# Kernel optimization log

Hardware: AMD Instinct MI355X
Metric: run time of the kernel (lower is better)

Reference implementation:

```python
import jax, jax.numpy as jnp
import numpy as np

N_NODES = 50000
N_EDGES = 800000
IN_FEATS = 128
HIDDEN = 96
NUM_CLASSES = 21
LEAKY_SLOPE = 0.01  # torch F.leaky_relu default


def setup_inputs() -> dict:
    key = jax.random.key(0)
    ks = jax.random.split(key, 12)
    x = jax.random.normal(ks[0], (N_NODES, IN_FEATS), dtype=jnp.float32)
    edge_index = jax.random.randint(ks[1], (2, N_EDGES), 0, N_NODES, dtype=jnp.int64)

    def glorot(k, fan_in, fan_out):
        lim = np.sqrt(6.0 / (fan_in + fan_out)).astype(np.float32)
        return jax.random.uniform(k, (fan_in, fan_out), jnp.float32, -lim, lim)

    return {
        "x": x,
        "edge_index": edge_index,
        "W1": glorot(ks[2], IN_FEATS, HIDDEN), "b1": jnp.zeros((HIDDEN,), jnp.float32),
        "W2": glorot(ks[3], HIDDEN, HIDDEN),   "b2": jnp.zeros((HIDDEN,), jnp.float32),
        "W3": glorot(ks[4], HIDDEN, HIDDEN),   "b3": jnp.zeros((HIDDEN,), jnp.float32),
        "Wl": glorot(ks[5], HIDDEN, NUM_CLASSES), "bl": jnp.zeros((NUM_CLASSES,), jnp.float32),
    }


def _gcn_norm(edge_index, num_nodes):
    # Add self-loops (PyG GCNConv default) and compute symmetric normalization
    loop = jnp.arange(num_nodes, dtype=edge_index.dtype)
    src = jnp.concatenate([edge_index[0], loop])  # source j
    tgt = jnp.concatenate([edge_index[1], loop])  # target i (aggregation index)
    ones = jnp.ones(src.shape[0], dtype=jnp.float32)
    deg = jax.ops.segment_sum(ones, tgt, num_segments=num_nodes)  # in-degree incl. self-loop
    dinv = jnp.where(deg > 0, jax.lax.rsqrt(deg), 0.0)
    norm = dinv[src] * dinv[tgt]  # [E+N]
    return src, tgt, norm


def _gcn_conv(h, src, tgt, norm, W, b, num_nodes):
    h = h @ W                                   # [N, out] dense transform first
    msg = norm[:, None] * h[src]                # gather + scale, [E+N, out]
    out = jax.ops.segment_sum(msg, tgt, num_segments=num_nodes)  # scatter-add
    return out + b


def reference(x, edge_index, W1, b1, W2, b2, W3, b3, Wl, bl):
    n = x.shape[0]
    src, tgt, norm = _gcn_norm(edge_index, n)
    # dropout is a no-op in eval mode (training=False)
    h = jax.nn.leaky_relu(_gcn_conv(x, src, tgt, norm, W1, b1, n), LEAKY_SLOPE)
    h = jax.nn.leaky_relu(_gcn_conv(h, src, tgt, norm, W2, b2, n), LEAKY_SLOPE)
    h = jax.nn.leaky_relu(_gcn_conv(h, src, tgt, norm, W3, b3, n), LEAKY_SLOPE)
    return h @ Wl + bl  # [N, num_classes]
```

## Files before the change

### kernel.cpp

```cpp
#include <hip/hip_runtime.h>
#include <hip/hip_fp16.h>

#define N_NODES 50000
#define N_EDGES 800000
#define IN_F 128
#define HID 96
#define NCLS 21
#define NBUCK 196
#define BCAP  4608
#define CPAD  16

typedef _Float16 hvec2 __attribute__((ext_vector_type(2)));

__device__ __forceinline__ float fdot2f(__half2 a, __half2 b, float c) {
#if __has_builtin(__builtin_amdgcn_fdot2)
  union { __half2 h; hvec2 v; } ua, ub;
  ua.h = a; ub.h = b;
  return __builtin_amdgcn_fdot2(ua.v, ub.v, c, false);
#else
  float2 fa = __half22float2(a), fb = __half22float2(b);
  return c + fa.x * fb.x + fa.y * fb.y;
#endif
}

__global__ void k_zero_int(int* __restrict__ p, int n) {
  int i = blockIdx.x * blockDim.x + threadIdx.x;
  if (i < n) p[i] = 0;
}

__global__ __launch_bounds__(1024) void k_bin(
    const int* __restrict__ src, const int* __restrict__ tgt,
    int* __restrict__ cursor, int* __restrict__ packed) {
  __shared__ int lhist[NBUCK];
  __shared__ int gbase[NBUCK];
  int tid = threadIdx.x;
  if (tid < NBUCK) lhist[tid] = 0;
  __syncthreads();
  int me = blockIdx.x * 4096 + tid * 4;
  int4 t4, s4;
  int b0 = 0, b1 = 0, b2 = 0, b3 = 0;
  bool valid = me < N_EDGES;
  if (valid) {
    t4 = *reinterpret_cast<const int4*>(tgt + me);
    s4 = *reinterpret_cast<const int4*>(src + me);
    b0 = t4.x >> 8; b1 = t4.y >> 8; b2 = t4.z >> 8; b3 = t4.w >> 8;
    atomicAdd(&lhist[b0], 1); atomicAdd(&lhist[b1], 1);
    atomicAdd(&lhist[b2], 1); atomicAdd(&lhist[b3], 1);
  }
  __syncthreads();
  if (tid < NBUCK) {
    int c = lhist[tid];
    gbase[tid] = c ? atomicAdd(&cursor[tid * CPAD], c) : 0;
    lhist[tid] = 0;
  }
  __syncthreads();
  if (valid) {
    int r, pos;
    r = atomicAdd(&lhist[b0], 1);
    pos = gbase[b0] + r;
    if (pos < BCAP) packed[b0 * BCAP + pos] = (s4.x << 8) | (t4.x & 255);
    r = atomicAdd(&lhist[b1], 1);
    pos = gbase[b1] + r;
    if (pos < BCAP) packed[b1 * BCAP + pos] = (s4.y << 8) | (t4.y & 255);
    r = atomicAdd(&lhist[b2], 1);
    pos = gbase[b2] + r;
    if (pos < BCAP) packed[b2 * BCAP + pos] = (s4.z << 8) | (t4.z & 255);
    r = atomicAdd(&lhist[b3], 1);
    pos = gbase[b3] + r;
    if (pos < BCAP) packed[b3 * BCAP + pos] = (s4.w << 8) | (t4.w & 255);
  }
}

__global__ __launch_bounds__(256) void k_build(
    const int* __restrict__ cursor, const int* __restrict__ packed,
    int* __restrict__ adj, int* __restrict__ degarr,
    int* __restrict__ rowptr, float* __restrict__ dinv) {
  __shared__ int ncnt[256];
  __shared__ int noff[256];
  __shared__ int nrank[256];
  __shared__ int ws[4];
  int b = blockIdx.x;
  int tid = threadIdx.x;
  int cntb = cursor[b * CPAD];
  if (cntb > BCAP) cntb = BCAP;
  ncnt[tid] = 0;
  nrank[tid] = 0;
  __syncthreads();
  const int* pk = packed + b * BCAP;
  for (int i = tid; i < cntb; i += 256) atomicAdd(&ncnt[pk[i] & 255], 1);
  __syncthreads();
  {
    int lane = tid & 63, wid = tid >> 6;
    int v = ncnt[tid];
    int x = v;
#pragma unroll
    for (int off = 1; off < 64; off <<= 1) {
      int y = __shfl_up(x, off);
      if (lane >= off) x += y;
    }
    if (lane == 63) ws[wid] = x;
    __syncthreads();
    if (tid == 0) {
      int t0 = ws[0], t1 = ws[1], t2 = ws[2];
      ws[3] = t0 + t1 + t2; ws[2] = t0 + t1; ws[1] = t0; ws[0] = 0;
    }
    __syncthreads();
    noff[tid] = ws[wid] + x - v;
  }
  __syncthreads();
  int n = (b << 8) + tid;
  if (n < N_NODES) {
    int d = ncnt[tid];
    degarr[n] = d;
    rowptr[n] = b * BCAP + noff[tid];
    dinv[n] = rsqrtf(1.0f + (float)d);
  }
  __syncthreads();
  for (int i = tid; i < cntb; i += 256) {
    int e = pk[i];
    int low = e & 255;
    int r = atomicAdd(&nrank[low], 1);
    adj[b * BCAP + noff[low] + r] = e >> 8;
  }
}

template<int K, bool A_HALF>
__global__ __launch_bounds__(128) void k_gemm_dot2(
    const void* __restrict__ Av, const float* __restrict__ W,
    const float* __restrict__ dinv, __half* __restrict__ g) {
  constexpr int BM = 64;
  constexpr int KP = 16;
  __shared__ __half2 As2[KP][BM + 2];
  __shared__ __half2 Ws2[KP][HID];
  int tid = threadIdx.x;
  int tx = tid & 15;
  int ty = tid >> 4;
  int f0 = tx * 6;
  int nbase = blockIdx.x * BM;
  float acc[8][6] = {};

  for (int k0 = 0; k0 < K; k0 += 32) {
    if (A_HALF) {
      const __half* A = (const __half*)Av;
#pragma unroll
      for (int i = 0; i < 2; i++) {
        int l = tid + i * 128;
        int row = l >> 2;
        int col8 = (l & 3) * 8;
        int n = nbase + row;
        uint4 v = make_uint4(0u, 0u, 0u, 0u);
        if (n < N_NODES)
          v = *reinterpret_cast<const uint4*>(A + (size_t)n * HID + k0 + col8);
        int p = col8 >> 1;
        As2[p + 0][row] = *(const __half2*)&v.x;
        As2[p + 1][row] = *(const __half2*)&v.y;
        As2[p + 2][row] = *(const __half2*)&v.z;
        As2[p + 3][row] = *(const __half2*)&v.w;
      }
    } else {
      const float* A = (const float*)Av;
#pragma unroll
      for (int i = 0; i < 4; i++) {
        int l = tid + i * 128;
        int row = l >> 3;
        int col = (l & 7) * 4;
        int n = nbase + row;
        float4 a4 = make_float4(0.f, 0.f, 0.f, 0.f);
        if (n < N_NODES)
          a4 = *reinterpret_cast<const float4*>(A + (size_t)n * K + k0 + col);
        As2[(col >> 1) + 0][row] = __floats2half2_rn(a4.x, a4.y);
        As2[(col >> 1) + 1][row] = __floats2half2_rn(a4.z, a4.w);
      }
    }
#pragma unroll
    for (int i = 0; i < 3; i++) {
      int l = tid + i * 128;
      int r2 = l / 24;
      int c4 = (l % 24) * 4;
      const float* w0 = W + (size_t)(k0 + 2 * r2) * HID + c4;
      float4 wa = *reinterpret_cast<const float4*>(w0);
      float4 wb = *reinterpret_cast<const float4*>(w0 + HID);
      Ws2[r2][c4 + 0] = __floats2half2_rn(wa.x, wb.x);
      Ws2[r2][c4 + 1] = __floats2half2_rn(wa.y, wb.y);
      Ws2[r2][c4 + 2] = __floats2half2_rn(wa.z, wb.z);
      Ws2[r2][c4 + 3] = __floats2half2_rn(wa.w, wb.w);
    }
    __syncthreads();
#pragma unroll
    for (int k2 = 0; k2 < KP; k2++) {
      __half2 av[8], wv[6];
#pragma unroll
      for (int i = 0; i < 8; i++) av[i] = As2[k2][ty * 8 + i];
#pragma unroll
      for (int j = 0; j < 6; j++) wv[j] = Ws2[k2][f0 + j];
#pragma unroll
      for (int i = 0; i < 8; i++)
#pragma unroll
        for (int j = 0; j < 6; j++) acc[i][j] = fdot2f(av[i], wv[j], acc[i][j]);
    }
    __syncthreads();
  }

#pragma unroll
  for (int i = 0; i < 8; i++) {
    int n = nbase + ty * 8 + i;
    if (n >= N_NODES) break;
    float d = dinv[n];
    __half2* gp = reinterpret_cast<__half2*>(g + (size_t)n * HID + f0);
#pragma unroll
    for (int j = 0; j < 3; j++)
      gp[j] = __floats2half2_rn(acc[i][2 * j] * d, acc[i][2 * j + 1] * d);
  }
}

__global__ __launch_bounds__(128) void k_aggregate(
    const __half* __restrict__ g, const int* __restrict__ degarr,
    const int* __restrict__ rowptr, const int* __restrict__ adj,
    const float* __restrict__ dinv, const float* __restrict__ b,
    __half* __restrict__ hout) {
  int n = blockIdx.x * 2 + (threadIdx.x >> 6);
  if (n >= N_NODES) return;
  int lane = threadIdx.x & 63;
  bool act = lane < 48;
  int deg = degarr[n];
  const int* al = adj + rowptr[n];
  int myidx = (lane < deg) ? al[lane] : 0;

  const char* gb = (const char*)g;
  int loff = lane * 4;
  float sx, sy;
  {
    unsigned v = act ? *(const unsigned*)(gb + (size_t)n * 192 + loff) : 0u;
    float2 t = __half22float2(*(const __half2*)&v);
    sx = t.x; sy = t.y;
  }

  int dd = deg > 64 ? 64 : deg;
  int j = 0;
  for (; j + 16 <= dd; j += 16) {
    unsigned v[16];
#pragma unroll
    for (int u = 0; u < 16; u++) {
      int idx = __shfl(myidx, j + u);
      v[u] = act ? *(const unsigned*)(gb + (size_t)idx * 192 + loff) : 0u;
    }
#pragma unroll
    for (int u = 0; u < 16; u++) {
      float2 t = __half22float2(*(const __half2*)&v[u]);
      sx += t.x; sy += t.y;
    }
  }
  if (j + 8 <= dd) {
    unsigned v[8];
#pragma unroll
    for (int u = 0; u < 8; u++) {
      int idx = __shfl(myidx, j + u);
      v[u] = act ? *(const unsigned*)(gb + (size_t)idx * 192 + loff) : 0u;
    }
#pragma unroll
    for (int u = 0; u < 8; u++) {
      float2 t = __half22float2(*(const __half2*)&v[u]);
      sx += t.x; sy += t.y;
    }
    j += 8;
  }
  if (j + 4 <= dd) {
    unsigned v[4];
#pragma unroll
    for (int u = 0; u < 4; u++) {
      int idx = __shfl(myidx, j + u);
      v[u] = act ? *(const unsigned*)(gb + (size_t)idx * 192 + loff) : 0u;
    }
#pragma unroll
    for (int u = 0; u < 4; u++) {
      float2 t = __half22float2(*(const __half2*)&v[u]);
      sx += t.x; sy += t.y;
    }
    j += 4;
  }
  for (; j < dd; j++) {
    int idx = __shfl(myidx, j);
    unsigned v = act ? *(const unsigned*)(gb + (size_t)idx * 192 + loff) : 0u;
    float2 t = __half22float2(*(const __half2*)&v);
    sx += t.x; sy += t.y;
  }
  for (; j < deg; j++) {
    int idx = al[j];
    unsigned v = act ? *(const unsigned*)(gb + (size_t)idx * 192 + loff) : 0u;
    float2 t = __half22float2(*(const __half2*)&v);
    sx += t.x; sy += t.y;
  }

  if (act) {
    float d = dinv[n];
    float2 bb = *reinterpret_cast<const float2*>(b + 2 * lane);
    float v0 = d * sx + bb.x;
    float v1 = d * sy + bb.y;
    v0 = v0 > 0.f ? v0 : 0.01f * v0;
    v1 = v1 > 0.f ? v1 : 0.01f * v1;
    *reinterpret_cast<__half2*>(hout + (size_t)n * HID + 2 * lane) =
        __floats2half2_rn(v0, v1);
  }
}

__global__ __launch_bounds__(256) void k_final(
    const __half* __restrict__ H, const float* __restrict__ Wl,
    const float* __restrict__ bl, float* __restrict__ out) {
  __shared__ __half2 w2[HID / 2][NCLS];
  __shared__ float bs[NCLS];
  int tid = threadIdx.x;
  for (int i = tid; i < (HID / 2) * NCLS; i += 256) {
    int r2 = i / NCLS;
    int c = i - r2 * NCLS;
    w2[r2][c] = __floats2half2_rn(Wl[(size_t)(2 * r2) * NCLS + c],
                                  Wl[(size_t)(2 * r2 + 1) * NCLS + c]);
  }
  if (tid < NCLS) bs[tid] = bl[tid];
  __syncthreads();
  int idx = blockIdx.x * 256 + tid;
  if (idx >= N_NODES * NCLS) return;
  int n = idx / NCLS;
  int c = idx - n * NCLS;
  const __half2* a2 = reinterpret_cast<const __half2*>(H + (size_t)n * HID);
  float s = bs[c];
#pragma unroll
  for (int k2 = 0; k2 < HID / 2; k2++) s = fdot2f(a2[k2], w2[k2][c], s);
  out[idx] = s;
}

extern "C" void kernel_launch(void* const* d_in, const int* in_sizes, int n_in,
                              void* d_out, int out_size, void* d_ws, size_t ws_size,
                              hipStream_t stream) {
  const float* x  = (const float*)d_in[0];
  const int* ei   = (const int*)d_in[1];
  const int* src  = ei;
  const int* tgt  = ei + N_EDGES;
  const float* W1 = (const float*)d_in[2];
  const float* b1 = (const float*)d_in[3];
  const float* W2 = (const float*)d_in[4];
  const float* b2 = (const float*)d_in[5];
  const float* W3 = (const float*)d_in[6];
  const float* b3 = (const float*)d_in[7];
  const float* Wl = (const float*)d_in[8];
  const float* bl = (const float*)d_in[9];
  float* out = (float*)d_out;

  float*  dinv   = (float*)d_ws;
  __half* bufG   = (__half*)(dinv + N_NODES);
  __half* bufH   = bufG + (size_t)N_NODES * HID;
  int*    degarr = (int*)(bufH + (size_t)N_NODES * HID);
  int*    rowptr = degarr + N_NODES;
  int*    cursor = rowptr + N_NODES;
  int*    packed = cursor + NBUCK * CPAD;
  int*    adj    = packed + NBUCK * BCAP;

  k_zero_int<<<(NBUCK * CPAD + 255) / 256, 256, 0, stream>>>(cursor, NBUCK * CPAD);
  k_bin<<<(N_EDGES + 4095) / 4096, 1024, 0, stream>>>(src, tgt, cursor, packed);
  k_build<<<NBUCK, 256, 0, stream>>>(cursor, packed, adj, degarr, rowptr, dinv);

  const int ggrid = (N_NODES + 63) / 64;
  const int agrid = (N_NODES + 1) / 2;

  k_gemm_dot2<IN_F, false><<<ggrid, 128, 0, stream>>>(x, W1, dinv, bufG);
  k_aggregate<<<agrid, 128, 0, stream>>>(bufG, degarr, rowptr, adj, dinv, b1, bufH);
  k_gemm_dot2<HID, true><<<ggrid, 128, 0, stream>>>(bufH, W2, dinv, bufG);
  k_aggregate<<<agrid, 128, 0, stream>>>(bufG, degarr, rowptr, adj, dinv, b2, bufH);
  k_gemm_dot2<HID, true><<<ggrid, 128, 0, stream>>>(bufH, W3, dinv, bufG);
  k_aggregate<<<agrid, 128, 0, stream>>>(bufG, degarr, rowptr, adj, dinv, b3, bufH);

  k_final<<<(N_NODES * NCLS + 255) / 256, 256, 0, stream>>>(bufH, Wl, bl, out);
}
```

Measured before the change: 196.4 us.

## Switch dense GEMM to MFMA f16 and use nontemporal gathers in aggregation

Replaces the packed-half dot2 GEMM with a 256-thread kernel in which each wave computes a 16-row tile using the 16x16x32 f16 MFMA across six column blocks, with A and transposed W staged in LDS. The aim is to move the dense transforms onto the matrix cores and cut their ALU time. The output stores become scattered 2-byte writes, and W is transposed with scalar loads on every k-step, which may add memory overhead. Neighbor gathers in the aggregation kernel also switch to nontemporal loads, which changes cache behaviour for a gather that is reused across many nodes and could hurt L2 reuse.

```diff
diff --git a/kernel.cpp b/kernel.cpp
--- a/kernel.cpp
+++ b/kernel.cpp
@@ -11,6 +11,8 @@
 #define CPAD  16
 
 typedef _Float16 hvec2 __attribute__((ext_vector_type(2)));
+typedef _Float16 f16x8 __attribute__((ext_vector_type(8)));
+typedef float f32x4 __attribute__((ext_vector_type(4)));
 
 __device__ __forceinline__ float fdot2f(__half2 a, __half2 b, float c) {
 #if __has_builtin(__builtin_amdgcn_fdot2)
@@ -125,91 +127,74 @@
 }
 
 template<int K, bool A_HALF>
-__global__ __launch_bounds__(128) void k_gemm_dot2(
+__global__ __launch_bounds__(256) void k_gemm_mfma(
     const void* __restrict__ Av, const float* __restrict__ W,
     const float* __restrict__ dinv, __half* __restrict__ g) {
   constexpr int BM = 64;
-  constexpr int KP = 16;
-  __shared__ __half2 As2[KP][BM + 2];
-  __shared__ __half2 Ws2[KP][HID];
+  constexpr int LDA = 40;
+  __shared__ _Float16 As[BM][LDA];
+  __shared__ _Float16 Wt[HID][LDA];
   int tid = threadIdx.x;
-  int tx = tid & 15;
-  int ty = tid >> 4;
-  int f0 = tx * 6;
+  int wave = tid >> 6;
+  int lane = tid & 63;
   int nbase = blockIdx.x * BM;
-  float acc[8][6] = {};
+  f32x4 acc[6] = {};
 
   for (int k0 = 0; k0 < K; k0 += 32) {
-    if (A_HALF) {
-      const __half* A = (const __half*)Av;
-#pragma unroll
-      for (int i = 0; i < 2; i++) {
-        int l = tid + i * 128;
-        int row = l >> 2;
-        int col8 = (l & 3) * 8;
-        int n = nbase + row;
+    {
+      int row = tid >> 2;
+      int c8 = (tid & 3) * 8;
+      int n = nbase + row;
+      if (A_HALF) {
+        const __half* A = (const __half*)Av;
         uint4 v = make_uint4(0u, 0u, 0u, 0u);
-        if (n < N_NODES)
-          v = *reinterpret_cast<const uint4*>(A + (size_t)n * HID + k0 + col8);
-        int p = col8 >> 1;
-        As2[p + 0][row] = *(const __half2*)&v.x;
-        As2[p + 1][row] = *(const __half2*)&v.y;
-        As2[p + 2][row] = *(const __half2*)&v.z;
-        As2[p + 3][row] = *(const __half2*)&v.w;
+        if (n < N_NODES) v = *reinterpret_cast<const uint4*>(A + (size_t)n * K + k0 + c8);
+        *reinterpret_cast<uint4*>(&As[row][c8]) = v;
+      } else {
+        const float* A = (const float*)Av;
+        float4 a0 = make_float4(0.f, 0.f, 0.f, 0.f), a1 = a0;
+        if (n < N_NODES) {
+          a0 = *reinterpret_cast<const float4*>(A + (size_t)n * K + k0 + c8);
+          a1 = *reinterpret_cast<const float4*>(A + (size_t)n * K + k0 + c8 + 4);
+        }
+        f16x8 hv;
+        hv[0] = (_Float16)a0.x; hv[1] = (_Float16)a0.y;
+        hv[2] = (_Float16)a0.z; hv[3] = (_Float16)a0.w;
+        hv[4] = (_Float16)a1.x; hv[5] = (_Float16)a1.y;
+        hv[6] = (_Float16)a1.z; hv[7] = (_Float16)a1.w;
+        *reinterpret_cast<f16x8*>(&As[row][c8]) = hv;
       }
-    } else {
-      const float* A = (const float*)Av;
-#pragma unroll
-      for (int i = 0; i < 4; i++) {
-        int l = tid + i * 128;
-        int row = l >> 3;
-        int col = (l & 7) * 4;
-        int n = nbase + row;
-        float4 a4 = make_float4(0.f, 0.f, 0.f, 0.f);
-        if (n < N_NODES)
-          a4 = *reinterpret_cast<const float4*>(A + (size_t)n * K + k0 + col);
-        As2[(col >> 1) + 0][row] = __floats2half2_rn(a4.x, a4.y);
-        As2[(col >> 1) + 1][row] = __floats2half2_rn(a4.z, a4.w);
+    }
+#pragma unroll
+    for (int i = 0; i < 12; i++) {
+      int idx = tid + i * 256;
+      int col = idx % HID;
+      int k = idx / HID;
+      Wt[col][k] = (_Float16)W[(size_t)(k0 + k) * HID + col];
+    }
+    __syncthreads();
+    {
+      f16x8 a = *reinterpret_cast<const f16x8*>(&As[wave * 16 + (lane & 15)][(lane >> 4) * 8]);
+#pragma unroll
+      for (int cb = 0; cb < 6; cb++) {
+        f16x8 b = *reinterpret_cast<const f16x8*>(&Wt[cb * 16 + (lane & 15)][(lane >> 4) * 8]);
+        acc[cb] = __builtin_amdgcn_mfma_f32_16x16x32_f16(a, b, acc[cb], 0, 0, 0);
       }
     }
-#pragma unroll
-    for (int i = 0; i < 3; i++) {
-      int l = tid + i * 128;
-      int r2 = l / 24;
-      int c4 = (l % 24) * 4;
-      const float* w0 = W + (size_t)(k0 + 2 * r2) * HID + c4;
-      float4 wa = *reinterpret_cast<const float4*>(w0);
-      float4 wb = *reinterpret_cast<const float4*>(w0 + HID);
-      Ws2[r2][c4 + 0] = __floats2half2_rn(wa.x, wb.x);
-      Ws2[r2][c4 + 1] = __floats2half2_rn(wa.y, wb.y);
-      Ws2[r2][c4 + 2] = __floats2half2_rn(wa.z, wb.z);
-      Ws2[r2][c4 + 3] = __floats2half2_rn(wa.w, wb.w);
-    }
     __syncthreads();
-#pragma unroll
-    for (int k2 = 0; k2 < KP; k2++) {
-      __half2 av[8], wv[6];
-#pragma unroll
-      for (int i = 0; i < 8; i++) av[i] = As2[k2][ty * 8 + i];
-#pragma unroll
-      for (int j = 0; j < 6; j++) wv[j] = Ws2[k2][f0 + j];
-#pragma unroll
-      for (int i = 0; i < 8; i++)
-#pragma unroll
-        for (int j = 0; j < 6; j++) acc[i][j] = fdot2f(av[i], wv[j], acc[i][j]);
-    }
-    __syncthreads();
-  }
-
-#pragma unroll
-  for (int i = 0; i < 8; i++) {
-    int n = nbase + ty * 8 + i;
-    if (n >= N_NODES) break;
-    float d = dinv[n];
-    __half2* gp = reinterpret_cast<__half2*>(g + (size_t)n * HID + f0);
-#pragma unroll
-    for (int j = 0; j < 3; j++)
-      gp[j] = __floats2half2_rn(acc[i][2 * j] * d, acc[i][2 * j + 1] * d);
+  }
+
+#pragma unroll
+  for (int r = 0; r < 4; r++) {
+    int row = wave * 16 + (lane >> 4) * 4 + r;
+    int n = nbase + row;
+    if (n < N_NODES) {
+      float d = dinv[n];
+      __half* gp = g + (size_t)n * HID + (lane & 15);
+#pragma unroll
+      for (int cb = 0; cb < 6; cb++)
+        gp[cb * 16] = __float2half(acc[cb][r] * d);
+    }
   }
 }
 
@@ -230,7 +215,8 @@
   int loff = lane * 4;
   float sx, sy;
   {
-    unsigned v = act ? *(const unsigned*)(gb + (size_t)n * 192 + loff) : 0u;
+    unsigned v = act ? __builtin_nontemporal_load(
+                           (const unsigned*)(gb + (size_t)n * 192 + loff)) : 0u;
     float2 t = __half22float2(*(const __half2*)&v);
     sx = t.x; sy = t.y;
   }
@@ -242,7 +228,8 @@
 #pragma unroll
     for (int u = 0; u < 16; u++) {
       int idx = __shfl(myidx, j + u);
-      v[u] = act ? *(const unsigned*)(gb + (size_t)idx * 192 + loff) : 0u;
+      v[u] = act ? __builtin_nontemporal_load(
+                       (const unsigned*)(gb + (size_t)idx * 192 + loff)) : 0u;
     }
 #pragma unroll
     for (int u = 0; u < 16; u++) {
@@ -255,7 +242,8 @@
 #pragma unroll
     for (int u = 0; u < 8; u++) {
       int idx = __shfl(myidx, j + u);
-      v[u] = act ? *(const unsigned*)(gb + (size_t)idx * 192 + loff) : 0u;
+      v[u] = act ? __builtin_nontemporal_load(
+                       (const unsigned*)(gb + (size_t)idx * 192 + loff)) : 0u;
     }
 #pragma unroll
     for (int u = 0; u < 8; u++) {
@@ -269,7 +257,8 @@
 #pragma unroll
     for (int u = 0; u < 4; u++) {
       int idx = __shfl(myidx, j + u);
-      v[u] = act ? *(const unsigned*)(gb + (size_t)idx * 192 + loff) : 0u;
+      v[u] = act ? __builtin_nontemporal_load(
+                       (const unsigned*)(gb + (size_t)idx * 192 + loff)) : 0u;
     }
 #pragma unroll
     for (int u = 0; u < 4; u++) {
@@ -280,13 +269,15 @@
   }
   for (; j < dd; j++) {
     int idx = __shfl(myidx, j);
-    unsigned v = act ? *(const unsigned*)(gb + (size_t)idx * 192 + loff) : 0u;
+    unsigned v = act ? __builtin_nontemporal_load(
+                           (const unsigned*)(gb + (size_t)idx * 192 + loff)) : 0u;
     float2 t = __half22float2(*(const __half2*)&v);
     sx += t.x; sy += t.y;
   }
   for (; j < deg; j++) {
     int idx = al[j];
-    unsigned v = act ? *(const unsigned*)(gb + (size_t)idx * 192 + loff) : 0u;
+    unsigned v = act ? __builtin_nontemporal_load(
+                           (const unsigned*)(gb + (size_t)idx * 192 + loff)) : 0u;
     float2 t = __half22float2(*(const __half2*)&v);
     sx += t.x; sy += t.y;
   }
@@ -361,11 +352,11 @@
   const int ggrid = (N_NODES + 63) / 64;
   const int agrid = (N_NODES + 1) / 2;
 
-  k_gemm_dot2<IN_F, false><<<ggrid, 128, 0, stream>>>(x, W1, dinv, bufG);
+  k_gemm_mfma<IN_F, false><<<ggrid, 256, 0, stream>>>(x, W1, dinv, bufG);
   k_aggregate<<<agrid, 128, 0, stream>>>(bufG, degarr, rowptr, adj, dinv, b1, bufH);
-  k_gemm_dot2<HID, true><<<ggrid, 128, 0, stream>>>(bufH, W2, dinv, bufG);
+  k_gemm_mfma<HID, true><<<ggrid, 256, 0, stream>>>(bufH, W2, dinv, bufG);
   k_aggregate<<<agrid, 128, 0, stream>>>(bufG, degarr, rowptr, adj, dinv, b2, bufH);
-  k_gemm_dot2<HID, true><<<ggrid, 128, 0, stream>>>(bufH, W3, dinv, bufG);
+  k_gemm_mfma<HID, true><<<ggrid, 256, 0, stream>>>(bufH, W3, dinv, bufG);
   k_aggregate<<<agrid, 128, 0, stream>>>(bufG, degarr, rowptr, adj, dinv, b3, bufH);
 
   k_final<<<(N_NODES * NCLS + 255) / 256, 256, 0, stream>>>(bufH, Wl, bl, out);
```

Measured after the change: 207.2 us. +5.5%, slower.
